# Optimization experiments

Hardware: AMD Instinct MI355X
Metric: run time of the kernel (lower is better)

## Reference

```python
import jax, jax.numpy as jnp
import numpy as np

N_IN, N_H = 512, 1024

def setup_inputs() -> dict:
    key = jax.random.key(0)
    ks = jax.random.split(key, 20)
    s_in = 1.0 / np.sqrt(N_IN)
    s_h = 1.0 / np.sqrt(N_H)
    inp = {
        'x': jax.random.normal(ks[0], (64, 256, N_IN), jnp.float32),
        'c': jax.random.normal(ks[1], (64, 256, N_H), jnp.float32),
        'h': jax.random.normal(ks[2], (64, 256, N_H), jnp.float32),
    }
    names_in = ['ii', 'if_', 'ig', 'io']
    names_h = ['hi', 'hf', 'hg', 'ho']
    k = 3
    for n in names_in:
        inp['W_' + n] = jax.random.uniform(ks[k], (N_H, N_IN), jnp.float32, -s_in, s_in); k += 1
        inp['b_' + n] = jax.random.uniform(ks[k], (N_H,), jnp.float32, -s_in, s_in); k += 1
    for n in names_h:
        inp['W_' + n] = jax.random.uniform(ks[k], (N_H, N_H), jnp.float32, -s_h, s_h); k += 1
        inp['b_' + n] = jax.random.uniform(ks[k], (N_H,), jnp.float32, -s_h, s_h); k += 1
    return inp

def reference(x, c, h,
              W_ii, b_ii, W_if_, b_if_, W_ig, b_ig, W_io, b_io,
              W_hi, b_hi, W_hf, b_hf, W_hg, b_hg, W_ho, b_ho):
    # Fuse the 4 input-side and 4 hidden-side linears into two GEMMs.
    Wx = jnp.concatenate([W_ii, W_if_, W_ig, W_io], axis=0)   # [4H, n_in]
    Wh = jnp.concatenate([W_hi, W_hf, W_hg, W_ho], axis=0)   # [4H, n_h]
    bx = jnp.concatenate([b_ii, b_if_, b_ig, b_io], axis=0)
    bh = jnp.concatenate([b_hi, b_hf, b_hg, b_ho], axis=0)
    z = jnp.einsum('sad,gd->sag', x, Wx) + jnp.einsum('sad,gd->sag', h, Wh) + bx + bh  # [S,A,4H]
    zi, zf, zg, zo = jnp.split(z, 4, axis=-1)
    i_t = jax.nn.sigmoid(zi)
    f_t = jax.nn.sigmoid(zf)
    g_t = jnp.tanh(zg)
    o_t = jax.nn.sigmoid(zo)
    c_t = f_t * c + i_t * g_t
    h_t = o_t * jnp.tanh(c_t)
    return (c_t, h_t)
```

## Files before the change

### kernel.cpp

```cpp
#include <hip/hip_runtime.h>
#include <hip/hip_bf16.h>

#define M_ROWS 16384
#define N_IN   512
#define N_HID  1024
#define K_TOT  1536
#define N_TOT  4096
#define NT     48

typedef __attribute__((ext_vector_type(4))) float f32x4;
typedef __attribute__((ext_vector_type(8))) short bf16x8;

__device__ __forceinline__ ushort f2bf(float f) {
    union { float f; unsigned u; } un; un.f = f;
    unsigned u = un.u;
    u += 0x7fffu + ((u >> 16) & 1u);
    return (ushort)(u >> 16);
}


__global__ void build_A(const float* __restrict__ x, const float* __restrict__ h,
                        ushort* __restrict__ A) {
    const int total = M_ROWS * K_TOT / 4;
    for (int p = blockIdx.x * blockDim.x + threadIdx.x; p < total;
         p += gridDim.x * blockDim.x) {
        int flat = p * 4;
        int row = flat / K_TOT;
        int col = flat - row * K_TOT;
        const float* src = (col < N_IN)
            ? (x + (size_t)row * N_IN + col)
            : (h + (size_t)row * N_HID + (col - N_IN));
        float4 v = *(const float4*)src;
        ushort4 o;
        o.x = f2bf(v.x); o.y = f2bf(v.y); o.z = f2bf(v.z); o.w = f2bf(v.w);
        *(ushort4*)(A + flat) = o;
    }
}

__global__ void build_W(const float* __restrict__ Wii, const float* __restrict__ Wif,
                        const float* __restrict__ Wig, const float* __restrict__ Wio,
                        const float* __restrict__ Whi, const float* __restrict__ Whf,
                        const float* __restrict__ Whg, const float* __restrict__ Who,
                        ushort* __restrict__ Wp) {
    const int total = N_TOT * K_TOT / 4;
    for (int p = blockIdx.x * blockDim.x + threadIdx.x; p < total;
         p += gridDim.x * blockDim.x) {
        int flat = p * 4;
        int prow = flat / K_TOT;
        int col = flat - prow * K_TOT;
        int bn  = prow >> 8;
        int r   = prow & 255;
        int wcn = r >> 6;
        int g   = (r >> 4) & 3;
        int u   = r & 15;
        int j   = bn * 64 + wcn * 16 + u;
        const float* src;
        if (col < N_IN) {
            const float* Wx = (g == 0) ? Wii : (g == 1) ? Wif : (g == 2) ? Wig : Wio;
            src = Wx + (size_t)j * N_IN + col;
        } else {
            const float* Wh = (g == 0) ? Whi : (g == 1) ? Whf : (g == 2) ? Whg : Who;
            src = Wh + (size_t)j * N_HID + (col - N_IN);
        }
        float4 v = *(const float4*)src;
        ushort4 o;
        o.x = f2bf(v.x); o.y = f2bf(v.y); o.z = f2bf(v.z); o.w = f2bf(v.w);
        *(ushort4*)(Wp + flat) = o;
    }
}

__global__ void build_bias(const float* __restrict__ bii, const float* __restrict__ bif,
                           const float* __restrict__ big, const float* __restrict__ bio,
                           const float* __restrict__ bhi, const float* __restrict__ bhf,
                           const float* __restrict__ bhg, const float* __restrict__ bho,
                           float* __restrict__ bias) {
    int n = blockIdx.x * blockDim.x + threadIdx.x;
    if (n >= N_TOT) return;
    int g = n >> 10, j = n & 1023;
    const float* bx = (g == 0) ? bii : (g == 1) ? bif : (g == 2) ? big : bio;
    const float* bh = (g == 0) ? bhi : (g == 1) ? bhf : (g == 2) ? bhg : bho;
    bias[n] = bx[j] + bh[j];
}


__device__ __forceinline__ float sigmoid_f(float z) {
    return 1.f / (1.f + __expf(-z));
}
__device__ __forceinline__ float tanh_f(float z) {
    z = fminf(fmaxf(z, -15.f), 15.f);
    float e = __expf(2.f * z);
    return (e - 1.f) / (e + 1.f);
}

__global__ __launch_bounds__(512, 1) void lstm_gemm(
        const ushort* __restrict__ A, const ushort* __restrict__ W,
        const float* __restrict__ bias, const float* __restrict__ cin,
        float* __restrict__ outc, float* __restrict__ outh) {
    __shared__ ushort sA[4][256 * 32];
    __shared__ ushort sB[4][256 * 32];

    const int tid  = threadIdx.x;
    const int wid  = tid >> 6;
    const int lane = tid & 63;
    const int wr  = wid >> 2;
    const int wcn = wid & 3;
    const int m0 = blockIdx.x * 256;
    const int n0 = blockIdx.y * 256;

    f32x4 acc[8][4] = {};

    const int srow = tid >> 2;
    const int fch  = (tid & 3) ^ ((tid >> 3) & 3);
    const ushort* gA = A + (size_t)(m0 + srow) * K_TOT + fch * 8;
    const ushort* gB = W + (size_t)(n0 + srow) * K_TOT + fch * 8;

#define GLDS(gptr, lptr) __builtin_amdgcn_global_load_lds(                     \
        (const __attribute__((address_space(1))) void*)(gptr),                 \
        (__attribute__((address_space(3))) void*)(lptr), 16, 0, 0)

#define STAGE(db, kt) do {                                                     \
    GLDS(gA + (size_t)(kt) * 32,                  &sA[db][tid * 8]);           \
    GLDS(gA + (size_t)128 * K_TOT + (size_t)(kt) * 32, &sA[db][4096 + tid * 8]); \
    GLDS(gB + (size_t)(kt) * 32,                  &sB[db][tid * 8]);           \
    GLDS(gB + (size_t)128 * K_TOT + (size_t)(kt) * 32, &sB[db][4096 + tid * 8]); \
} while (0)

    const int lrow = lane & 15;
    const int cb0  = lane >> 4;
    const int csw2 = (lrow >> 1) & 3;
    const int koff = ((cb0 ^ csw2) * 8);
    const int aBase = (wr * 128 + lrow) * 32 + koff;
    const int bBase = (wcn * 64 + lrow) * 32 + koff;

#define READS(afX, bfX, db) do {                                               \
    _Pragma("unroll")                                                          \
    for (int m = 0; m < 8; ++m)                                                \
        afX[m] = *(const bf16x8*)&sA[db][aBase + m * 512];                     \
    _Pragma("unroll")                                                          \
    for (int n = 0; n < 4; ++n)                                                \
        bfX[n] = *(const bf16x8*)&sB[db][bBase + n * 512];                     \
} while (0)

#define MFMAS(afX, bfX) do {                                                   \
    __builtin_amdgcn_s_setprio(1);                                             \
    _Pragma("unroll")                                                          \
    for (int m = 0; m < 8; ++m)                                                \
        _Pragma("unroll")                                                      \
        for (int n = 0; n < 4; ++n)                                            \
            acc[m][n] = __builtin_amdgcn_mfma_f32_16x16x32_bf16(               \
                afX[m], bfX[n], acc[m][n], 0, 0, 0);                           \
    __builtin_amdgcn_s_setprio(0);                                             \
} while (0)

#define BARX() __builtin_amdgcn_s_barrier()
#define VMC(n) asm volatile("s_waitcnt vmcnt(" #n ")" ::: "memory")

    bf16x8 af0[8], bfv0[4], af1[8], bfv1[4];

    STAGE(0, 0); STAGE(1, 1); STAGE(2, 2);
    VMC(4);
    BARX();
    READS(af0, bfv0, 0);

#define TILE(u, t, Fna, Fnb, Fca, Fcb) do {                                    \
    STAGE(((u) + 3) & 3, (t) + 3);                                             \
    READS(Fna, Fnb, ((u) + 1) & 3);                                            \
    MFMAS(Fca, Fcb);                                                           \
    VMC(4);                                                                    \
    BARX();                                                                    \
} while (0)

    for (int hh = 0; hh < 11; ++hh) {
        const int t = hh * 4;
        TILE(0, t + 0, af1, bfv1, af0, bfv0);
        TILE(1, t + 1, af0, bfv0, af1, bfv1);
        TILE(2, t + 2, af1, bfv1, af0, bfv0);
        TILE(3, t + 3, af0, bfv0, af1, bfv1);
    }
    TILE(0, 44, af1, bfv1, af0, bfv0);
    READS(af0, bfv0, 2);
    MFMAS(af1, bfv1);
    VMC(0);
    BARX();
    READS(af1, bfv1, 3);
    MFMAS(af0, bfv0);
    BARX();
    MFMAS(af1, bfv1);

    const int unit = blockIdx.y * 64 + wcn * 16 + lrow;
    const float b0 = bias[unit];
    const float b1 = bias[1024 + unit];
    const float b2 = bias[2048 + unit];
    const float b3 = bias[3072 + unit];
    const int r0 = m0 + wr * 128 + (lane >> 4) * 4;
#pragma unroll
    for (int mi = 0; mi < 8; ++mi) {
#pragma unroll
        for (int q = 0; q < 4; ++q) {
            const int row = r0 + mi * 16 + q;
            const size_t off = (size_t)row * N_HID + unit;
            float zi = acc[mi][0][q] + b0;
            float zf = acc[mi][1][q] + b1;
            float zg = acc[mi][2][q] + b2;
            float zo = acc[mi][3][q] + b3;
            float it_ = sigmoid_f(zi);
            float ft = sigmoid_f(zf);
            float gt = tanh_f(zg);
            float ot = sigmoid_f(zo);
            float ct = ft * cin[off] + it_ * gt;
            float ht = ot * tanh_f(ct);
            outc[off] = ct;
            outh[off] = ht;
        }
    }
#undef GLDS
#undef STAGE
#undef READS
#undef MFMAS
#undef BARX
#undef VMC
#undef TILE
}


extern "C" void kernel_launch(void* const* d_in, const int* in_sizes, int n_in,
                              void* d_out, int out_size, void* d_ws, size_t ws_size,
                              hipStream_t stream) {
    const float* x = (const float*)d_in[0];
    const float* c = (const float*)d_in[1];
    const float* h = (const float*)d_in[2];
    const float* Wii = (const float*)d_in[3];  const float* bii = (const float*)d_in[4];
    const float* Wif = (const float*)d_in[5];  const float* bif = (const float*)d_in[6];
    const float* Wig = (const float*)d_in[7];  const float* big = (const float*)d_in[8];
    const float* Wio = (const float*)d_in[9];  const float* bio = (const float*)d_in[10];
    const float* Whi = (const float*)d_in[11]; const float* bhi = (const float*)d_in[12];
    const float* Whf = (const float*)d_in[13]; const float* bhf = (const float*)d_in[14];
    const float* Whg = (const float*)d_in[15]; const float* bhg = (const float*)d_in[16];
    const float* Who = (const float*)d_in[17]; const float* bho = (const float*)d_in[18];

    char* ws = (char*)d_ws;
    ushort* A_cat  = (ushort*)ws;
    ushort* W_perm = (ushort*)(ws + (size_t)M_ROWS * K_TOT * 2);
    float*  biasc  = (float*)(ws + (size_t)M_ROWS * K_TOT * 2
                                 + (size_t)N_TOT * K_TOT * 2);

    float* outc = (float*)d_out;
    float* outh = (float*)d_out + (size_t)M_ROWS * N_HID;

    hipLaunchKernelGGL(build_A, dim3(2048), dim3(256), 0, stream, x, h, A_cat);
    hipLaunchKernelGGL(build_W, dim3(1024), dim3(256), 0, stream,
                       Wii, Wif, Wig, Wio, Whi, Whf, Whg, Who, W_perm);
    hipLaunchKernelGGL(build_bias, dim3(16), dim3(256), 0, stream,
                       bii, bif, big, bio, bhi, bhf, bhg, bho, biasc);
    hipLaunchKernelGGL(lstm_gemm, dim3(M_ROWS / 256, N_TOT / 256), dim3(512), 0, stream,
                       A_cat, W_perm, biasc, c, outc, outh);
}
```

Before: 286.1 us.

## Switch LSTM GEMM to 32x32x16 MFMA with 4x2 wave tiling and inline LDS reads

Replaces the 16x16x32 bf16 MFMA tiling (2x4 waves, 8x4 accumulators of 4 floats) with 32x32x16 MFMAs on a 4x2 wave layout (2x4 accumulators of 16 floats). The weight packing is reordered so each wave's 32-column gate group lines up with the new fragment layout. LDS fragment loads become inline-asm ds_read_b128 with immediate offsets and explicit lgkmcnt waits. The intent is fewer MFMA issues and LDS reads per FLOP and tighter control of the schedule, at the cost of fragile hand-managed waitcounts and possible register pressure.

New measurement: 295.4 us. 3.2% more time.

```diff
diff --git a/kernel.cpp b/kernel.cpp
--- a/kernel.cpp
+++ b/kernel.cpp
@@ -8,14 +8,19 @@
 #define N_TOT  4096
 #define NT     48
 
-typedef __attribute__((ext_vector_type(4))) float f32x4;
-typedef __attribute__((ext_vector_type(8))) short bf16x8;
+typedef __attribute__((ext_vector_type(16))) float f32x16;
+typedef __attribute__((ext_vector_type(8)))  short bf16x8;
+typedef __attribute__((ext_vector_type(4)))  int   i32x4;
 
 __device__ __forceinline__ ushort f2bf(float f) {
     union { float f; unsigned u; } un; un.f = f;
     unsigned u = un.u;
     u += 0x7fffu + ((u >> 16) & 1u);
     return (ushort)(u >> 16);
+}
+
+__device__ __forceinline__ bf16x8 as_bf(i32x4 v) {
+    union { i32x4 i; bf16x8 b; } u; u.i = v; return u.b;
 }
 
 
@@ -50,10 +55,10 @@
         int col = flat - prow * K_TOT;
         int bn  = prow >> 8;
         int r   = prow & 255;
-        int wcn = r >> 6;
-        int g   = (r >> 4) & 3;
-        int u   = r & 15;
-        int j   = bn * 64 + wcn * 16 + u;
+        int wc  = r >> 7;
+        int g   = (r >> 5) & 3;
+        int u   = r & 31;
+        int j   = bn * 64 + wc * 32 + u;
         const float* src;
         if (col < N_IN) {
             const float* Wx = (g == 0) ? Wii : (g == 1) ? Wif : (g == 2) ? Wig : Wio;
@@ -102,12 +107,12 @@
     const int tid  = threadIdx.x;
     const int wid  = tid >> 6;
     const int lane = tid & 63;
-    const int wr  = wid >> 2;
-    const int wcn = wid & 3;
+    const int wr  = wid >> 1;
+    const int wc  = wid & 1;
     const int m0 = blockIdx.x * 256;
     const int n0 = blockIdx.y * 256;
 
-    f32x4 acc[8][4] = {};
+    f32x16 acc[2][4] = {};
 
     const int srow = tid >> 2;
     const int fch  = (tid & 3) ^ ((tid >> 3) & 3);
@@ -119,90 +124,115 @@
         (__attribute__((address_space(3))) void*)(lptr), 16, 0, 0)
 
 #define STAGE(db, kt) do {                                                     \
-    GLDS(gA + (size_t)(kt) * 32,                  &sA[db][tid * 8]);           \
+    GLDS(gA + (size_t)(kt) * 32,                       &sA[db][tid * 8]);      \
     GLDS(gA + (size_t)128 * K_TOT + (size_t)(kt) * 32, &sA[db][4096 + tid * 8]); \
-    GLDS(gB + (size_t)(kt) * 32,                  &sB[db][tid * 8]);           \
+    GLDS(gB + (size_t)(kt) * 32,                       &sB[db][tid * 8]);      \
     GLDS(gB + (size_t)128 * K_TOT + (size_t)(kt) * 32, &sB[db][4096 + tid * 8]); \
 } while (0)
 
-    const int lrow = lane & 15;
-    const int cb0  = lane >> 4;
-    const int csw2 = (lrow >> 1) & 3;
-    const int koff = ((cb0 ^ csw2) * 8);
-    const int aBase = (wr * 128 + lrow) * 32 + koff;
-    const int bBase = (wcn * 64 + lrow) * 32 + koff;
+    const int r31 = lane & 31;
+    const int khl = lane >> 5;
+    const int csw = (r31 >> 1) & 3;
+    const unsigned aOff0 = (unsigned)((wr * 64  + r31) * 64 + ((0 * 2 + khl) ^ csw) * 16);
+    const unsigned aOff1 = (unsigned)((wr * 64  + r31) * 64 + ((1 * 2 + khl) ^ csw) * 16);
+    const unsigned bOff0 = (unsigned)((wc * 128 + r31) * 64 + ((0 * 2 + khl) ^ csw) * 16);
+    const unsigned bOff1 = (unsigned)((wc * 128 + r31) * 64 + ((1 * 2 + khl) ^ csw) * 16);
+
+#define DSR(dst, addr, IMM) asm volatile(                                      \
+    "ds_read_b128 %0, %1 offset:" IMM : "=&v"(dst) : "v"(addr))
 
 #define READS(afX, bfX, db) do {                                               \
-    _Pragma("unroll")                                                          \
-    for (int m = 0; m < 8; ++m)                                                \
-        afX[m] = *(const bf16x8*)&sA[db][aBase + m * 512];                     \
-    _Pragma("unroll")                                                          \
-    for (int n = 0; n < 4; ++n)                                                \
-        bfX[n] = *(const bf16x8*)&sB[db][bBase + n * 512];                     \
+    unsigned aB_ = (unsigned)(uintptr_t)                                       \
+        (__attribute__((address_space(3))) ushort*)&sA[db][0];                 \
+    unsigned bB_ = (unsigned)(uintptr_t)                                       \
+        (__attribute__((address_space(3))) ushort*)&sB[db][0];                 \
+    unsigned a0_ = aB_ + aOff0, a1_ = aB_ + aOff1;                             \
+    unsigned b0_ = bB_ + bOff0, b1_ = bB_ + bOff1;                             \
+    DSR(afX[0][0], a0_, "0");  DSR(afX[1][0], a0_, "2048");                    \
+    DSR(afX[0][1], a1_, "0");  DSR(afX[1][1], a1_, "2048");                    \
+    DSR(bfX[0][0], b0_, "0");  DSR(bfX[1][0], b0_, "2048");                    \
+    DSR(bfX[2][0], b0_, "4096"); DSR(bfX[3][0], b0_, "6144");                  \
+    DSR(bfX[0][1], b1_, "0");  DSR(bfX[1][1], b1_, "2048");                    \
+    DSR(bfX[2][1], b1_, "4096"); DSR(bfX[3][1], b1_, "6144");                  \
+} while (0)
+
+#define WAITK(n) do {                                                          \
+    asm volatile("s_waitcnt lgkmcnt(" #n ")");                                 \
+    __builtin_amdgcn_sched_barrier(0);                                         \
 } while (0)
 
 #define MFMAS(afX, bfX) do {                                                   \
     __builtin_amdgcn_s_setprio(1);                                             \
     _Pragma("unroll")                                                          \
-    for (int m = 0; m < 8; ++m)                                                \
+    for (int mi = 0; mi < 2; ++mi)                                             \
         _Pragma("unroll")                                                      \
-        for (int n = 0; n < 4; ++n)                                            \
-            acc[m][n] = __builtin_amdgcn_mfma_f32_16x16x32_bf16(               \
-                afX[m], bfX[n], acc[m][n], 0, 0, 0);                           \
+        for (int g = 0; g < 4; ++g)                                            \
+            acc[mi][g] = __builtin_amdgcn_mfma_f32_32x32x16_bf16(              \
+                as_bf(afX[mi][0]), as_bf(bfX[g][0]), acc[mi][g], 0, 0, 0);     \
+    _Pragma("unroll")                                                          \
+    for (int mi = 0; mi < 2; ++mi)                                             \
+        _Pragma("unroll")                                                      \
+        for (int g = 0; g < 4; ++g)                                            \
+            acc[mi][g] = __builtin_amdgcn_mfma_f32_32x32x16_bf16(              \
+                as_bf(afX[mi][1]), as_bf(bfX[g][1]), acc[mi][g], 0, 0, 0);     \
     __builtin_amdgcn_s_setprio(0);                                             \
 } while (0)
 
 #define BARX() __builtin_amdgcn_s_barrier()
 #define VMC(n) asm volatile("s_waitcnt vmcnt(" #n ")" ::: "memory")
 
-    bf16x8 af0[8], bfv0[4], af1[8], bfv1[4];
+    i32x4 af0[2][2], bf0[4][2], af1[2][2], bf1[4][2];
 
     STAGE(0, 0); STAGE(1, 1); STAGE(2, 2);
     VMC(4);
     BARX();
-    READS(af0, bfv0, 0);
-
-#define TILE(u, t, Fna, Fnb, Fca, Fcb) do {                                    \
+    READS(af0, bf0, 0);
+
+#define TILE(u, t, FnA, FnB, FcA, FcB) do {                                    \
     STAGE(((u) + 3) & 3, (t) + 3);                                             \
-    READS(Fna, Fnb, ((u) + 1) & 3);                                            \
-    MFMAS(Fca, Fcb);                                                           \
+    READS(FnA, FnB, ((u) + 1) & 3);                                            \
+    WAITK(12);                                                                 \
+    MFMAS(FcA, FcB);                                                           \
     VMC(4);                                                                    \
     BARX();                                                                    \
 } while (0)
 
     for (int hh = 0; hh < 11; ++hh) {
         const int t = hh * 4;
-        TILE(0, t + 0, af1, bfv1, af0, bfv0);
-        TILE(1, t + 1, af0, bfv0, af1, bfv1);
-        TILE(2, t + 2, af1, bfv1, af0, bfv0);
-        TILE(3, t + 3, af0, bfv0, af1, bfv1);
-    }
-    TILE(0, 44, af1, bfv1, af0, bfv0);
-    READS(af0, bfv0, 2);
-    MFMAS(af1, bfv1);
+        TILE(0, t + 0, af1, bf1, af0, bf0);
+        TILE(1, t + 1, af0, bf0, af1, bf1);
+        TILE(2, t + 2, af1, bf1, af0, bf0);
+        TILE(3, t + 3, af0, bf0, af1, bf1);
+    }
+    TILE(0, 44, af1, bf1, af0, bf0);
+    READS(af0, bf0, 2);
+    WAITK(12);
+    MFMAS(af1, bf1);
     VMC(0);
     BARX();
-    READS(af1, bfv1, 3);
-    MFMAS(af0, bfv0);
+    READS(af1, bf1, 3);
+    WAITK(12);
+    MFMAS(af0, bf0);
     BARX();
-    MFMAS(af1, bfv1);
-
-    const int unit = blockIdx.y * 64 + wcn * 16 + lrow;
+    WAITK(0);
+    MFMAS(af1, bf1);
+
+    const int unit = blockIdx.y * 64 + wc * 32 + r31;
     const float b0 = bias[unit];
     const float b1 = bias[1024 + unit];
     const float b2 = bias[2048 + unit];
     const float b3 = bias[3072 + unit];
-    const int r0 = m0 + wr * 128 + (lane >> 4) * 4;
+    const int r0 = m0 + wr * 64 + 4 * khl;
 #pragma unroll
-    for (int mi = 0; mi < 8; ++mi) {
+    for (int mi = 0; mi < 2; ++mi) {
 #pragma unroll
-        for (int q = 0; q < 4; ++q) {
-            const int row = r0 + mi * 16 + q;
+        for (int reg = 0; reg < 16; ++reg) {
+            const int row = r0 + mi * 32 + (reg & 3) + 8 * (reg >> 2);
             const size_t off = (size_t)row * N_HID + unit;
-            float zi = acc[mi][0][q] + b0;
-            float zf = acc[mi][1][q] + b1;
-            float zg = acc[mi][2][q] + b2;
-            float zo = acc[mi][3][q] + b3;
+            float zi = acc[mi][0][reg] + b0;
+            float zf = acc[mi][1][reg] + b1;
+            float zg = acc[mi][2][reg] + b2;
+            float zo = acc[mi][3][reg] + b3;
             float it_ = sigmoid_f(zi);
             float ft = sigmoid_f(zf);
             float gt = tanh_f(zg);
@@ -215,7 +245,9 @@
     }
 #undef GLDS
 #undef STAGE
+#undef DSR
 #undef READS
+#undef WAITK
 #undef MFMAS
 #undef BARX
 #undef VMC
```

## Shrink GEMM tile to 128x128 with 4 waves, two blocks per CU, inline-asm LDS reads

Applied to the files above, without the earlier changes.

The fused LSTM GEMM block tile drops from 256x256 with 8 waves to 128x128 with 4 waves, and launch bounds now allow two blocks per CU. The weight permutation is changed to match the new per-wave gate layout. LDS fragment loads become explicit ds_read_b128 with immediate offsets, and an lgkmcnt wait plus sched_barrier is placed before each MFMA batch so reads overlap with compute. The aim is more occupancy and latency hiding, at the cost of less data reuse per tile and more global/L2 traffic.

Measured after the change: 311.1 us. 8.7% more time.

```diff
diff --git a/kernel.cpp b/kernel.cpp
--- a/kernel.cpp
+++ b/kernel.cpp
@@ -10,12 +10,17 @@
 
 typedef __attribute__((ext_vector_type(4))) float f32x4;
 typedef __attribute__((ext_vector_type(8))) short bf16x8;
+typedef __attribute__((ext_vector_type(4))) int   i32x4;
 
 __device__ __forceinline__ ushort f2bf(float f) {
     union { float f; unsigned u; } un; un.f = f;
     unsigned u = un.u;
     u += 0x7fffu + ((u >> 16) & 1u);
     return (ushort)(u >> 16);
+}
+
+__device__ __forceinline__ bf16x8 as_bf(i32x4 v) {
+    union { i32x4 i; bf16x8 b; } u; u.i = v; return u.b;
 }
 
 
@@ -48,12 +53,13 @@
         int flat = p * 4;
         int prow = flat / K_TOT;
         int col = flat - prow * K_TOT;
-        int bn  = prow >> 8;
-        int r   = prow & 255;
-        int wcn = r >> 6;
-        int g   = (r >> 4) & 3;
-        int u   = r & 15;
-        int j   = bn * 64 + wcn * 16 + u;
+        int grp = prow >> 7;
+        int tt = prow & 127;
+        int cc = (tt >> 6) & 1;
+        int ss = tt & 63;
+        int g  = ss >> 4;
+        int u  = ss & 15;
+        int j  = grp * 32 + cc * 16 + u;
         const float* src;
         if (col < N_IN) {
             const float* Wx = (g == 0) ? Wii : (g == 1) ? Wif : (g == 2) ? Wig : Wio;
@@ -92,22 +98,22 @@
     return (e - 1.f) / (e + 1.f);
 }
 
-__global__ __launch_bounds__(512, 1) void lstm_gemm(
+__global__ __launch_bounds__(256, 2) void lstm_gemm(
         const ushort* __restrict__ A, const ushort* __restrict__ W,
         const float* __restrict__ bias, const float* __restrict__ cin,
         float* __restrict__ outc, float* __restrict__ outh) {
-    __shared__ ushort sA[4][256 * 32];
-    __shared__ ushort sB[4][256 * 32];
+    __shared__ ushort sA[4][128 * 32];
+    __shared__ ushort sB[4][128 * 32];
 
     const int tid  = threadIdx.x;
     const int wid  = tid >> 6;
     const int lane = tid & 63;
-    const int wr  = wid >> 2;
-    const int wcn = wid & 3;
-    const int m0 = blockIdx.x * 256;
-    const int n0 = blockIdx.y * 256;
-
-    f32x4 acc[8][4] = {};
+    const int wr = wid >> 1;
+    const int wc = wid & 1;
+    const int m0 = blockIdx.x * 128;
+    const int n0 = blockIdx.y * 128;
+
+    f32x4 acc[4][4] = {};
 
     const int srow = tid >> 2;
     const int fch  = (tid & 3) ^ ((tid >> 3) & 3);
@@ -119,82 +125,95 @@
         (__attribute__((address_space(3))) void*)(lptr), 16, 0, 0)
 
 #define STAGE(db, kt) do {                                                     \
-    GLDS(gA + (size_t)(kt) * 32,                  &sA[db][tid * 8]);           \
-    GLDS(gA + (size_t)128 * K_TOT + (size_t)(kt) * 32, &sA[db][4096 + tid * 8]); \
-    GLDS(gB + (size_t)(kt) * 32,                  &sB[db][tid * 8]);           \
-    GLDS(gB + (size_t)128 * K_TOT + (size_t)(kt) * 32, &sB[db][4096 + tid * 8]); \
+    GLDS(gA + (size_t)(kt) * 32,                      &sA[db][tid * 8]);       \
+    GLDS(gA + (size_t)64 * K_TOT + (size_t)(kt) * 32, &sA[db][2048 + tid * 8]); \
+    GLDS(gB + (size_t)(kt) * 32,                      &sB[db][tid * 8]);       \
+    GLDS(gB + (size_t)64 * K_TOT + (size_t)(kt) * 32, &sB[db][2048 + tid * 8]); \
 } while (0)
 
     const int lrow = lane & 15;
     const int cb0  = lane >> 4;
-    const int csw2 = (lrow >> 1) & 3;
-    const int koff = ((cb0 ^ csw2) * 8);
-    const int aBase = (wr * 128 + lrow) * 32 + koff;
-    const int bBase = (wcn * 64 + lrow) * 32 + koff;
+    const int csw  = (lrow >> 1) & 3;
+    const unsigned aByte = (unsigned)(((wr * 64 + lrow) * 32 + ((cb0 ^ csw) * 8)) * 2);
+    const unsigned bByte = (unsigned)(((wc * 64 + lrow) * 32 + ((cb0 ^ csw) * 8)) * 2);
+
+#define DSR(dst, addr, IMM) asm volatile(                                      \
+    "ds_read_b128 %0, %1 offset:" IMM : "=&v"(dst) : "v"(addr))
 
 #define READS(afX, bfX, db) do {                                               \
-    _Pragma("unroll")                                                          \
-    for (int m = 0; m < 8; ++m)                                                \
-        afX[m] = *(const bf16x8*)&sA[db][aBase + m * 512];                     \
-    _Pragma("unroll")                                                          \
-    for (int n = 0; n < 4; ++n)                                                \
-        bfX[n] = *(const bf16x8*)&sB[db][bBase + n * 512];                     \
+    unsigned aAd = (unsigned)(uintptr_t)                                       \
+        (__attribute__((address_space(3))) ushort*)&sA[db][0] + aByte;         \
+    unsigned bAd = (unsigned)(uintptr_t)                                       \
+        (__attribute__((address_space(3))) ushort*)&sB[db][0] + bByte;         \
+    DSR(afX[0], aAd, "0");    DSR(afX[1], aAd, "1024");                        \
+    DSR(afX[2], aAd, "2048"); DSR(afX[3], aAd, "3072");                        \
+    DSR(bfX[0], bAd, "0");    DSR(bfX[1], bAd, "1024");                        \
+    DSR(bfX[2], bAd, "2048"); DSR(bfX[3], bAd, "3072");                        \
+} while (0)
+
+#define WAITK(n) do {                                                          \
+    asm volatile("s_waitcnt lgkmcnt(" #n ")");                                 \
+    __builtin_amdgcn_sched_barrier(0);                                         \
 } while (0)
 
 #define MFMAS(afX, bfX) do {                                                   \
     __builtin_amdgcn_s_setprio(1);                                             \
     _Pragma("unroll")                                                          \
-    for (int m = 0; m < 8; ++m)                                                \
+    for (int m = 0; m < 4; ++m)                                                \
         _Pragma("unroll")                                                      \
         for (int n = 0; n < 4; ++n)                                            \
             acc[m][n] = __builtin_amdgcn_mfma_f32_16x16x32_bf16(               \
-                afX[m], bfX[n], acc[m][n], 0, 0, 0);                           \
+                as_bf(afX[m]), as_bf(bfX[n]), acc[m][n], 0, 0, 0);             \
     __builtin_amdgcn_s_setprio(0);                                             \
 } while (0)
 
 #define BARX() __builtin_amdgcn_s_barrier()
 #define VMC(n) asm volatile("s_waitcnt vmcnt(" #n ")" ::: "memory")
 
-    bf16x8 af0[8], bfv0[4], af1[8], bfv1[4];
+    i32x4 af0[4], bf0[4], af1[4], bf1[4];
 
     STAGE(0, 0); STAGE(1, 1); STAGE(2, 2);
     VMC(4);
     BARX();
-    READS(af0, bfv0, 0);
-
-#define TILE(u, t, Fna, Fnb, Fca, Fcb) do {                                    \
+    READS(af0, bf0, 0);
+
+#define TILE(u, t, FnA, FnB, FcA, FcB) do {                                    \
     STAGE(((u) + 3) & 3, (t) + 3);                                             \
-    READS(Fna, Fnb, ((u) + 1) & 3);                                            \
-    MFMAS(Fca, Fcb);                                                           \
+    READS(FnA, FnB, ((u) + 1) & 3);                                            \
+    WAITK(8);                                                                  \
+    MFMAS(FcA, FcB);                                                           \
     VMC(4);                                                                    \
     BARX();                                                                    \
 } while (0)
 
     for (int hh = 0; hh < 11; ++hh) {
         const int t = hh * 4;
-        TILE(0, t + 0, af1, bfv1, af0, bfv0);
-        TILE(1, t + 1, af0, bfv0, af1, bfv1);
-        TILE(2, t + 2, af1, bfv1, af0, bfv0);
-        TILE(3, t + 3, af0, bfv0, af1, bfv1);
-    }
-    TILE(0, 44, af1, bfv1, af0, bfv0);
-    READS(af0, bfv0, 2);
-    MFMAS(af1, bfv1);
+        TILE(0, t + 0, af1, bf1, af0, bf0);
+        TILE(1, t + 1, af0, bf0, af1, bf1);
+        TILE(2, t + 2, af1, bf1, af0, bf0);
+        TILE(3, t + 3, af0, bf0, af1, bf1);
+    }
+    TILE(0, 44, af1, bf1, af0, bf0);
+    READS(af0, bf0, 2);
+    WAITK(8);
+    MFMAS(af1, bf1);
     VMC(0);
     BARX();
-    READS(af1, bfv1, 3);
-    MFMAS(af0, bfv0);
+    READS(af1, bf1, 3);
+    WAITK(8);
+    MFMAS(af0, bf0);
     BARX();
-    MFMAS(af1, bfv1);
-
-    const int unit = blockIdx.y * 64 + wcn * 16 + lrow;
+    WAITK(0);
+    MFMAS(af1, bf1);
+
+    const int unit = blockIdx.y * 32 + wc * 16 + lrow;
     const float b0 = bias[unit];
     const float b1 = bias[1024 + unit];
     const float b2 = bias[2048 + unit];
     const float b3 = bias[3072 + unit];
-    const int r0 = m0 + wr * 128 + (lane >> 4) * 4;
+    const int r0 = m0 + wr * 64 + (lane >> 4) * 4;
 #pragma unroll
-    for (int mi = 0; mi < 8; ++mi) {
+    for (int mi = 0; mi < 4; ++mi) {
 #pragma unroll
         for (int q = 0; q < 4; ++q) {
             const int row = r0 + mi * 16 + q;
@@ -215,7 +234,9 @@
     }
 #undef GLDS
 #undef STAGE
+#undef DSR
 #undef READS
+#undef WAITK
 #undef MFMAS
 #undef BARX
 #undef VMC
@@ -252,6 +273,6 @@
                        Wii, Wif, Wig, Wio, Whi, Whf, Whg, Who, W_perm);
     hipLaunchKernelGGL(build_bias, dim3(16), dim3(256), 0, stream,
                        bii, bif, big, bio, bhi, bhf, bhg, bho, biasc);
-    hipLaunchKernelGGL(lstm_gemm, dim3(M_ROWS / 256, N_TOT / 256), dim3(512), 0, stream,
+    hipLaunchKernelGGL(lstm_gemm, dim3(M_ROWS / 128, N_TOT / 128), dim3(256), 0, stream,
                        A_cat, W_perm, biasc, c, outc, outh);
 }
```
